# Optimization experiments

Hardware: AMD Instinct MI355X
Metric: run time of the kernel (lower is better)

Reference implementation:

```python
import jax, jax.numpy as jnp
import numpy as np

B, S, D = 4, 2048, 1024

def setup_inputs() -> dict:
    key = jax.random.key(0)
    k1, k2, k3, k4 = jax.random.split(key, 4)
    scale = 1.0 / np.sqrt(D)
    return {
        "X": jax.random.normal(k1, (B, S, D), dtype=jnp.float32),
        "W_Q": jax.random.normal(k2, (D, D), dtype=jnp.float32) * scale,
        "W_K": jax.random.normal(k3, (D, D), dtype=jnp.float32) * scale,
        "W_V": jax.random.normal(k4, (D, D), dtype=jnp.float32) * scale,
    }

def reference(X, W_Q, W_K, W_V):
    # nn.Linear computes X @ W.T; weights stored as [out, in]
    Q = jnp.einsum('bsd,ed->bse', X, W_Q)
    K = jnp.einsum('bsd,ed->bse', X, W_K)
    V = jnp.einsum('bsd,ed->bse', X, W_V)
    d_model = X.shape[-1]
    scores = jnp.einsum('bqd,bkd->bqk', Q, K) / jnp.sqrt(jnp.float32(d_model))
    S_len = X.shape[1]
    causal = jnp.tril(jnp.ones((S_len, S_len), dtype=bool))  # True = keep
    scores = jnp.where(causal[None, :, :], scores, -jnp.inf)
    attn = jax.nn.softmax(scores, axis=-1)
    return jnp.einsum('bqk,bkd->bqd', attn, V)
```

## Files before the change

kernel.cpp:

```cpp
#include <hip/hip_runtime.h>

typedef unsigned short u16;
typedef __attribute__((ext_vector_type(8))) short short8;
typedef __attribute__((ext_vector_type(4))) float floatx4;
typedef __attribute__((ext_vector_type(4))) unsigned short ushortx4;

#define BATCH 4
#define SEQ   2048
#define DMODEL 1024

__device__ __forceinline__ u16 f2bf(float f) {
  unsigned int u = __builtin_bit_cast(unsigned int, f);
  u = (u + 0x7FFFu + ((u >> 16) & 1u)) >> 16;
  return (u16)u;
}

typedef const __attribute__((address_space(1))) unsigned int as1_u32;
typedef __attribute__((address_space(3))) unsigned int as3_u32;

__device__ __forceinline__ void gload16(const void* gp, void* lp) {
  __builtin_amdgcn_global_load_lds((as1_u32*)gp, (as3_u32*)lp, 16, 0, 0);
}

#define CFENCE asm volatile("" ::: "memory")
#define LGKM0  do { asm volatile("s_waitcnt lgkmcnt(0)" ::: "memory"); \
                    __builtin_amdgcn_sched_barrier(0); } while (0)
#define VMC(n) asm volatile("s_waitcnt vmcnt(" #n ")" ::: "memory")
#define BAR    __builtin_amdgcn_s_barrier()
#define PRIO1  __builtin_amdgcn_s_setprio(1)
#define PRIO0  __builtin_amdgcn_s_setprio(0)

template<int NW, int STRIPE>
__device__ __forceinline__ void stage_unit(
    const u16* __restrict__ G, int ld, int org, int kt, int h,
    u16* region, int w, int l)
{
  constexpr int CPS = STRIPE / 16;
  const int lr = l >> 3, s = l & 7;
  #pragma unroll
  for (int i = 0; i < 2; ++i) {
    int c = i * NW + w;
    int R = (c / CPS) * STRIPE + h * (STRIPE / 2) + (c % CPS) * 8;
    const u16* src = G + (size_t)(org + R + lr) * ld + kt * 64 + ((s ^ lr) << 3);
    gload16(src, region + R * 64);
  }
}

template<int REP>
__device__ __forceinline__ short8 rdfrag(const u16* region, int wq, int m, int kh, int l) {
  int r = wq * (REP * 16) + m * 16 + (l & 15);
  int c = kh * 32 + ((l >> 4) << 3);
  return *(const short8*)(region + ((r * 64 + c) ^ ((r & 7) << 3)));
}

template<int WM, int WN, int MREP, int NREP>
__device__ __forceinline__ void gemm_core(
    const u16* __restrict__ A, int lda,
    const u16* __restrict__ B, int ldb,
    int m0, int n0, int NT, u16* lds,
    floatx4 (&acc)[MREP][NREP])
{
  constexpr int NW = WM * WN;
  constexpr int BM = WM * MREP * 16, BN = WN * NREP * 16;
  constexpr int ABUF = BM * 64;
  constexpr int BUFSZ = (BM + BN) * 64;
  constexpr int MH = MREP / 2, NH = NREP / 2;
  constexpr int SA = BM / WM, SB = BN / WN;

  const int tid = threadIdx.x;
  const int w = tid >> 6, l = tid & 63;
  const int wr = w / WN, wc = w % WN;

  u16* const bufp[2] = { lds, lds + BUFSZ };

  stage_unit<NW, SA>(A, lda, m0, 0, 0, bufp[0], w, l);
  stage_unit<NW, SB>(B, ldb, n0, 0, 0, bufp[0] + ABUF, w, l);
  stage_unit<NW, SB>(B, ldb, n0, 0, 1, bufp[0] + ABUF, w, l);
  stage_unit<NW, SA>(A, lda, m0, 0, 1, bufp[0], w, l);
  stage_unit<NW, SA>(A, lda, m0, 1, 0, bufp[1], w, l);
  stage_unit<NW, SB>(B, ldb, n0, 1, 0, bufp[1] + ABUF, w, l);
  stage_unit<NW, SB>(B, ldb, n0, 1, 1, bufp[1] + ABUF, w, l);
  VMC(6);
  BAR;
  CFENCE;

  for (int t = 0; t < NT; t += 2) {
    u16* c0 = bufp[t & 1];
    u16* c1 = bufp[(t + 1) & 1];
    const int t2 = (t + 2 < NT) ? t + 2 : NT - 1;
    const int t3 = (t + 3 < NT) ? t + 3 : NT - 1;

    short8 aLo[MH][2], aHi[MH][2], bLo[NH][2], bHi[NH][2];

    #pragma unroll
    for (int m = 0; m < MH; ++m)
      #pragma unroll
      for (int k = 0; k < 2; ++k) aLo[m][k] = rdfrag<MREP>(c0, wr, m, k, l);
    #pragma unroll
    for (int n = 0; n < NH; ++n)
      #pragma unroll
      for (int k = 0; k < 2; ++k) bLo[n][k] = rdfrag<NREP>(c0 + ABUF, wc, n, k, l);
    stage_unit<NW, SA>(A, lda, m0, t + 1, 1, c1, w, l);
    if constexpr (MH * 2 + NH * 2 >= 12) asm volatile("s_waitcnt lgkmcnt(8)" ::: "memory");
    BAR; LGKM0; PRIO1;
    #pragma unroll
    for (int m = 0; m < MH; ++m)
      #pragma unroll
      for (int n = 0; n < NH; ++n)
        #pragma unroll
        for (int k = 0; k < 2; ++k)
          acc[m][n] = __builtin_amdgcn_mfma_f32_16x16x32_bf16(aLo[m][k], bLo[n][k], acc[m][n], 0, 0, 0);
    PRIO0; BAR; CFENCE;

    #pragma unroll
    for (int n = 0; n < NH; ++n)
      #pragma unroll
      for (int k = 0; k < 2; ++k) bHi[n][k] = rdfrag<NREP>(c0 + ABUF, wc, n + NH, k, l);
    stage_unit<NW, SA>(A, lda, m0, t2, 0, c0, w, l);
    BAR; LGKM0; PRIO1;
    #pragma unroll
    for (int m = 0; m < MH; ++m)
      #pragma unroll
      for (int n = 0; n < NH; ++n)
        #pragma unroll
        for (int k = 0; k < 2; ++k)
          acc[m][n + NH] = __builtin_amdgcn_mfma_f32_16x16x32_bf16(aLo[m][k], bHi[n][k], acc[m][n + NH], 0, 0, 0);
    PRIO0; BAR; CFENCE;

    #pragma unroll
    for (int m = 0; m < MH; ++m)
      #pragma unroll
      for (int k = 0; k < 2; ++k) aHi[m][k] = rdfrag<MREP>(c0, wr, m + MH, k, l);
    stage_unit<NW, SB>(B, ldb, n0, t2, 0, c0 + ABUF, w, l);
    BAR; LGKM0; PRIO1;
    #pragma unroll
    for (int m = 0; m < MH; ++m)
      #pragma unroll
      for (int n = 0; n < NH; ++n)
        #pragma unroll
        for (int k = 0; k < 2; ++k)
          acc[m + MH][n + NH] = __builtin_amdgcn_mfma_f32_16x16x32_bf16(aHi[m][k], bHi[n][k], acc[m + MH][n + NH], 0, 0, 0);
    PRIO0; BAR; CFENCE;

    stage_unit<NW, SB>(B, ldb, n0, t2, 1, c0 + ABUF, w, l);
    VMC(6);
    BAR; PRIO1;
    #pragma unroll
    for (int m = 0; m < MH; ++m)
      #pragma unroll
      for (int n = 0; n < NH; ++n)
        #pragma unroll
        for (int k = 0; k < 2; ++k)
          acc[m + MH][n] = __builtin_amdgcn_mfma_f32_16x16x32_bf16(aHi[m][k], bLo[n][k], acc[m + MH][n], 0, 0, 0);
    PRIO0; BAR; CFENCE;

    #pragma unroll
    for (int m = 0; m < MH; ++m)
      #pragma unroll
      for (int k = 0; k < 2; ++k) aLo[m][k] = rdfrag<MREP>(c1, wr, m, k, l);
    #pragma unroll
    for (int n = 0; n < NH; ++n)
      #pragma unroll
      for (int k = 0; k < 2; ++k) bLo[n][k] = rdfrag<NREP>(c1 + ABUF, wc, n, k, l);
    stage_unit<NW, SA>(A, lda, m0, t2, 1, c0, w, l);
    if constexpr (MH * 2 + NH * 2 >= 12) asm volatile("s_waitcnt lgkmcnt(8)" ::: "memory");
    BAR; LGKM0; PRIO1;
    #pragma unroll
    for (int m = 0; m < MH; ++m)
      #pragma unroll
      for (int n = 0; n < NH; ++n)
        #pragma unroll
        for (int k = 0; k < 2; ++k)
          acc[m][n] = __builtin_amdgcn_mfma_f32_16x16x32_bf16(aLo[m][k], bLo[n][k], acc[m][n], 0, 0, 0);
    PRIO0; BAR; CFENCE;

    #pragma unroll
    for (int n = 0; n < NH; ++n)
      #pragma unroll
      for (int k = 0; k < 2; ++k) bHi[n][k] = rdfrag<NREP>(c1 + ABUF, wc, n + NH, k, l);
    stage_unit<NW, SA>(A, lda, m0, t3, 0, c1, w, l);
    BAR; LGKM0; PRIO1;
    #pragma unroll
    for (int m = 0; m < MH; ++m)
      #pragma unroll
      for (int n = 0; n < NH; ++n)
        #pragma unroll
        for (int k = 0; k < 2; ++k)
          acc[m][n + NH] = __builtin_amdgcn_mfma_f32_16x16x32_bf16(aLo[m][k], bHi[n][k], acc[m][n + NH], 0, 0, 0);
    PRIO0; BAR; CFENCE;

    #pragma unroll
    for (int m = 0; m < MH; ++m)
      #pragma unroll
      for (int k = 0; k < 2; ++k) aHi[m][k] = rdfrag<MREP>(c1, wr, m + MH, k, l);
    stage_unit<NW, SB>(B, ldb, n0, t3, 0, c1 + ABUF, w, l);
    BAR; LGKM0; PRIO1;
    #pragma unroll
    for (int m = 0; m < MH; ++m)
      #pragma unroll
      for (int n = 0; n < NH; ++n)
        #pragma unroll
        for (int k = 0; k < 2; ++k)
          acc[m + MH][n + NH] = __builtin_amdgcn_mfma_f32_16x16x32_bf16(aHi[m][k], bHi[n][k], acc[m + MH][n + NH], 0, 0, 0);
    PRIO0; BAR; CFENCE;

    stage_unit<NW, SB>(B, ldb, n0, t3, 1, c1 + ABUF, w, l);
    VMC(6);
    BAR; PRIO1;
    #pragma unroll
    for (int m = 0; m < MH; ++m)
      #pragma unroll
      for (int n = 0; n < NH; ++n)
        #pragma unroll
        for (int k = 0; k < 2; ++k)
          acc[m + MH][n] = __builtin_amdgcn_mfma_f32_16x16x32_bf16(aHi[m][k], bLo[n][k], acc[m + MH][n], 0, 0, 0);
    PRIO0; BAR; CFENCE;
  }
  VMC(0);
}

__global__ __launch_bounds__(256)
void convert_k(const float* __restrict__ X,
               const float* __restrict__ WQ,
               const float* __restrict__ WK,
               const float* __restrict__ WV,
               u16* __restrict__ Xb, u16* __restrict__ Wb)
{
  const int NX = (BATCH*SEQ*DMODEL) / 4;
  const int NW_ = (DMODEL*DMODEL) / 4;
  const int total = NX + 3*NW_;
  for (int i = blockIdx.x * 256 + threadIdx.x; i < total; i += gridDim.x * 256) {
    const float4* src; u16* dst; int j;
    if (i < NX) { src = (const float4*)X; j = i; dst = Xb; }
    else {
      int t = i - NX; int w = t / NW_; j = t - w * NW_;
      src = (const float4*)(w == 0 ? WQ : (w == 1 ? WK : WV));
      dst = Wb + (size_t)w * (DMODEL*DMODEL);
    }
    float4 v = src[j];
    ushortx4 p = { f2bf(v.x), f2bf(v.y), f2bf(v.z), f2bf(v.w) };
    *(ushortx4*)(dst + (size_t)j * 4) = p;
  }
}

__global__ __launch_bounds__(512, 2)
void qk256(const u16* __restrict__ Xb, const u16* __restrict__ Wb,
           u16* __restrict__ Q, u16* __restrict__ K)
{
  __shared__ __align__(16) u16 lds[2 * (256 + 256) * 64];
  const int id = blockIdx.x;
  const int sw = (id & 7) * 32 + (id >> 3);
  const int z = sw >> 7;
  const int rem = sw & 127;
  const int mt = rem >> 2, nt = rem & 3;
  const int m0 = mt * 256, n0 = nt * 256;

  floatx4 acc[8][4] = {};
  gemm_core<2, 4, 8, 4>(Xb, DMODEL, Wb + (size_t)z * DMODEL * DMODEL, DMODEL,
                        m0, n0, DMODEL / 64, lds, acc);

  const int l = threadIdx.x & 63, w = threadIdx.x >> 6;
  const int wr = w >> 2, wc = w & 3;
  const int row0 = m0 + wr * 128 + ((l >> 4) << 2);
  const int col0 = n0 + wc * 64 + (l & 15);
  u16* O = z ? K : Q;
  #pragma unroll
  for (int m = 0; m < 8; ++m)
    #pragma unroll
    for (int n = 0; n < 4; ++n)
      #pragma unroll
      for (int i = 0; i < 4; ++i)
        O[(size_t)(row0 + m*16 + i) * DMODEL + col0 + n*16] = f2bf(acc[m][n][i]);
}

__global__ __launch_bounds__(256, 2)
void v128(const u16* __restrict__ Xb, const u16* __restrict__ Wb,
          u16* __restrict__ Vt)
{
  __shared__ __align__(16) u16 lds[2 * (128 + 128) * 64];
  const int id = blockIdx.x;
  const int sw = (id & 7) * 64 + (id >> 3);
  const int mt = sw >> 3, nt = sw & 7;
  const int m0 = mt * 128, n0 = nt * 128;

  floatx4 acc[4][4] = {};
  gemm_core<2, 2, 4, 4>(Xb, DMODEL, Wb + (size_t)2 * DMODEL * DMODEL, DMODEL,
                        m0, n0, DMODEL / 64, lds, acc);

  const int l = threadIdx.x & 63, w = threadIdx.x >> 6;
  const int wr = w >> 1, wc = w & 1;
  const int row0 = m0 + wr * 64 + ((l >> 4) << 2);
  const int col0 = n0 + wc * 64 + (l & 15);
  #pragma unroll
  for (int m = 0; m < 4; ++m) {
    int gm = row0 + m*16;
    int b = gm >> 11, s = gm & (SEQ - 1);
    #pragma unroll
    for (int n = 0; n < 4; ++n) {
      int d = col0 + n*16;
      ushortx4 p = { f2bf(acc[m][n][0]), f2bf(acc[m][n][1]),
                     f2bf(acc[m][n][2]), f2bf(acc[m][n][3]) };
      *(ushortx4*)(Vt + ((size_t)b * DMODEL + d) * SEQ + s) = p;
    }
  }
}

__global__ __launch_bounds__(256, 2)
void scores128(const u16* __restrict__ Qb, const u16* __restrict__ Kb,
               float* __restrict__ Sc)
{
  __shared__ __align__(16) u16 lds[2 * (128 + 128) * 64];
  const int id = blockIdx.x;
  const int sw = (id & 7) * 68 + (id >> 3);
  const int b = sw / 136;
  const int t = sw % 136;
  int qt = 0;
  while ((qt + 1) * (qt + 2) / 2 <= t) ++qt;
  const int kt = t - qt * (qt + 1) / 2;
  const int m0 = qt * 128, n0 = kt * 128;

  const u16* Q = Qb + (size_t)b * SEQ * DMODEL;
  const u16* K = Kb + (size_t)b * SEQ * DMODEL;
  floatx4 acc[4][4] = {};
  gemm_core<2, 2, 4, 4>(Q, DMODEL, K, DMODEL, m0, n0, DMODEL / 64, lds, acc);

  float* S = Sc + (size_t)b * SEQ * SEQ;
  const int l = threadIdx.x & 63, w = threadIdx.x >> 6;
  const int wr = w >> 1, wc = w & 1;
  const int row0 = m0 + wr * 64 + ((l >> 4) << 2);
  const int col0 = n0 + wc * 64 + (l & 15);
  #pragma unroll
  for (int m = 0; m < 4; ++m)
    #pragma unroll
    for (int n = 0; n < 4; ++n)
      #pragma unroll
      for (int i = 0; i < 4; ++i)
        S[(size_t)(row0 + m*16 + i) * SEQ + col0 + n*16] = acc[m][n][i] * 0.03125f;
}

__global__ __launch_bounds__(256)
void softmax_k(float* __restrict__ Sc)
{
  __shared__ float buf[SEQ];
  __shared__ float red[4];
  const int rg = blockIdx.x;
  const int q = rg & (SEQ - 1);
  float* row = Sc + (size_t)rg * SEQ;
  u16* prow = (u16*)row;
  const int tid = threadIdx.x;
  const int lane = tid & 63, wave = tid >> 6;
  const int n = q + 1;
  const int kpad = ((q >> 8) + 1) << 8;

  float lmax = -3.4e38f;
  for (int k = tid; k < n; k += 256) {
    float v = row[k];
    buf[k] = v;
    lmax = fmaxf(lmax, v);
  }
  #pragma unroll
  for (int off = 32; off >= 1; off >>= 1)
    lmax = fmaxf(lmax, __shfl_xor(lmax, off));
  if (lane == 0) red[wave] = lmax;
  __syncthreads();
  const float rmax = fmaxf(fmaxf(red[0], red[1]), fmaxf(red[2], red[3]));
  __syncthreads();

  float lsum = 0.f;
  for (int k = tid; k < n; k += 256) {
    float e = __expf(buf[k] - rmax);
    buf[k] = e;
    lsum += e;
  }
  #pragma unroll
  for (int off = 32; off >= 1; off >>= 1)
    lsum += __shfl_xor(lsum, off);
  if (lane == 0) red[wave] = lsum;
  __syncthreads();
  const float inv = 1.f / (red[0] + red[1] + red[2] + red[3]);

  for (int k = tid; k < kpad; k += 256) {
    float p = (k < n) ? buf[k] * inv : 0.f;
    prow[k] = f2bf(p);
  }
}

__global__ __launch_bounds__(256, 2)
void out128(const float* __restrict__ Sc, const u16* __restrict__ Vt,
            float* __restrict__ Out)
{
  __shared__ __align__(16) u16 lds[2 * (128 + 128) * 64];
  const int id = blockIdx.x;
  const int j = id & 255;
  const int upper = id >> 8;
  const int qt = upper ? (15 - (j & 15)) : (j & 15);
  const int nt = (j >> 4) & 7;
  const int b  = (upper << 1) | (j >> 7);
  const int m0 = qt * 128, n0 = nt * 128;

  const u16* P = (const u16*)(Sc + (size_t)b * SEQ * SEQ);
  const u16* V = Vt + (size_t)b * DMODEL * SEQ;
  const int NT = (qt + 1) * 2;

  floatx4 acc[4][4] = {};
  gemm_core<2, 2, 4, 4>(P, 2 * SEQ, V, SEQ, m0, n0, NT, lds, acc);

  float* O = Out + (size_t)b * SEQ * DMODEL;
  const int l = threadIdx.x & 63, w = threadIdx.x >> 6;
  const int wr = w >> 1, wc = w & 1;
  const int row0 = m0 + wr * 64 + ((l >> 4) << 2);
  const int col0 = n0 + wc * 64 + (l & 15);
  #pragma unroll
  for (int m = 0; m < 4; ++m)
    #pragma unroll
    for (int n = 0; n < 4; ++n)
      #pragma unroll
      for (int i = 0; i < 4; ++i)
        O[(size_t)(row0 + m*16 + i) * DMODEL + col0 + n*16] = acc[m][n][i];
}

extern "C" void kernel_launch(void* const* d_in, const int* in_sizes, int n_in,
                              void* d_out, int out_size, void* d_ws, size_t ws_size,
                              hipStream_t stream)
{
  const float* X  = (const float*)d_in[0];
  const float* WQ = (const float*)d_in[1];
  const float* WK = (const float*)d_in[2];
  const float* WV = (const float*)d_in[3];
  float* Out = (float*)d_out;

  char* ws = (char*)d_ws;
  u16*   Xb = (u16*)(ws);
  u16*   Wb = (u16*)(ws + 16777216);
  u16*   Qb = (u16*)(ws + 23068672);
  u16*   Kb = (u16*)(ws + 39845888);
  u16*   Vt = (u16*)(ws + 56623104);
  float* Sc = (float*)(ws + 73400320);

  convert_k<<<dim3(2048), dim3(256), 0, stream>>>(X, WQ, WK, WV, Xb, Wb);
  qk256<<<dim3(256), dim3(512), 0, stream>>>(Xb, Wb, Qb, Kb);
  v128<<<dim3(512), dim3(256), 0, stream>>>(Xb, Wb, Vt);
  scores128<<<dim3(544), dim3(256), 0, stream>>>(Qb, Kb, Sc);
  softmax_k<<<dim3(BATCH * SEQ), dim3(256), 0, stream>>>(Sc);
  out128<<<dim3(512), dim3(256), 0, stream>>>(Sc, Vt, Out);
}
```

Before: 145.2 us.

## Merge V projection with scores GEMM, store scores in bf16, single-pass softmax

Merges the V projection and QK^T scores GEMMs into one launch of 1056 blocks, so they share a grid and one launch is removed. Scores are now written as bf16 instead of fp32, which halves the score-matrix traffic into and out of softmax. Softmax loads one 8-element vector per thread into registers instead of staging through LDS, and pads the causal row to 128 instead of 256. The QK projection switches to a new three-phase gemm_core variant with finer-grained prefetch and barriers. Rounding scores to bf16 before softmax lowers precision.

```diff
diff --git a/kernel.cpp b/kernel.cpp
--- a/kernel.cpp
+++ b/kernel.cpp
@@ -13,6 +13,10 @@
   unsigned int u = __builtin_bit_cast(unsigned int, f);
   u = (u + 0x7FFFu + ((u >> 16) & 1u)) >> 16;
   return (u16)u;
+}
+__device__ __forceinline__ float bf2f(u16 u) {
+  unsigned int v = ((unsigned int)u) << 16;
+  return __builtin_bit_cast(float, v);
 }
 
 typedef const __attribute__((address_space(1))) unsigned int as1_u32;
@@ -54,7 +58,113 @@
 }
 
 template<int WM, int WN, int MREP, int NREP>
-__device__ __forceinline__ void gemm_core(
+__device__ __forceinline__ void gemm_core3(
+    const u16* __restrict__ A, int lda,
+    const u16* __restrict__ B, int ldb,
+    int m0, int n0, int NT, u16* lds,
+    floatx4 (&acc)[MREP][NREP])
+{
+  constexpr int NW = WM * WN;
+  constexpr int BM = WM * MREP * 16, BN = WN * NREP * 16;
+  constexpr int ABUF = BM * 64;
+  constexpr int BUFSZ = (BM + BN) * 64;
+  constexpr int MH = MREP / 2, NH = NREP / 2;
+  constexpr int SA = BM / WM, SB = BN / WN;
+
+  const int tid = threadIdx.x;
+  const int w = tid >> 6, l = tid & 63;
+  const int wr = w / WN, wc = w % WN;
+
+  u16* buf0 = lds;
+  u16* buf1 = lds + BUFSZ;
+
+  stage_unit<NW, SA>(A, lda, m0, 0, 0, buf0, w, l);
+  stage_unit<NW, SB>(B, ldb, n0, 0, 0, buf0 + ABUF, w, l);
+  stage_unit<NW, SB>(B, ldb, n0, 0, 1, buf0 + ABUF, w, l);
+  stage_unit<NW, SA>(A, lda, m0, 0, 1, buf0, w, l);
+  stage_unit<NW, SA>(A, lda, m0, 1, 0, buf1, w, l);
+  stage_unit<NW, SB>(B, ldb, n0, 1, 0, buf1 + ABUF, w, l);
+  VMC(8);
+  BAR;
+  CFENCE;
+
+  for (int kt = 0; kt < NT; ++kt) {
+    u16* cur = (kt & 1) ? buf1 : buf0;
+    u16* oth = (kt & 1) ? buf0 : buf1;
+    const int t1 = (kt + 1 < NT) ? kt + 1 : NT - 1;
+    const int t2 = (kt + 2 < NT) ? kt + 2 : NT - 1;
+
+    short8 aLo[MH][2], aHi[MH][2], bLo[NH][2], bHi[NH][2];
+
+    #pragma unroll
+    for (int m = 0; m < MH; ++m)
+      #pragma unroll
+      for (int k = 0; k < 2; ++k) aLo[m][k] = rdfrag<MREP>(cur, wr, m, k, l);
+    #pragma unroll
+    for (int n = 0; n < NH; ++n)
+      #pragma unroll
+      for (int k = 0; k < 2; ++k) bLo[n][k] = rdfrag<NREP>(cur + ABUF, wc, n, k, l);
+    stage_unit<NW, SB>(B, ldb, n0, t1, 1, oth + ABUF, w, l);
+    stage_unit<NW, SA>(A, lda, m0, t1, 1, oth, w, l);
+    VMC(10);
+    LGKM0;
+    BAR;
+    CFENCE;
+    PRIO1;
+    #pragma unroll
+    for (int m = 0; m < MH; ++m)
+      #pragma unroll
+      for (int n = 0; n < NH; ++n)
+        #pragma unroll
+        for (int k = 0; k < 2; ++k)
+          acc[m][n] = __builtin_amdgcn_mfma_f32_16x16x32_bf16(aLo[m][k], bLo[n][k], acc[m][n], 0, 0, 0);
+    PRIO0;
+
+    #pragma unroll
+    for (int n = 0; n < NH; ++n)
+      #pragma unroll
+      for (int k = 0; k < 2; ++k) bHi[n][k] = rdfrag<NREP>(cur + ABUF, wc, n + NH, k, l);
+    stage_unit<NW, SA>(A, lda, m0, t2, 0, cur, w, l);
+    VMC(10);
+    LGKM0;
+    BAR;
+    CFENCE;
+    PRIO1;
+    #pragma unroll
+    for (int m = 0; m < MH; ++m)
+      #pragma unroll
+      for (int n = 0; n < NH; ++n)
+        #pragma unroll
+        for (int k = 0; k < 2; ++k)
+          acc[m][n + NH] = __builtin_amdgcn_mfma_f32_16x16x32_bf16(aLo[m][k], bHi[n][k], acc[m][n + NH], 0, 0, 0);
+    PRIO0;
+
+    #pragma unroll
+    for (int m = 0; m < MH; ++m)
+      #pragma unroll
+      for (int k = 0; k < 2; ++k) aHi[m][k] = rdfrag<MREP>(cur, wr, m + MH, k, l);
+    stage_unit<NW, SB>(B, ldb, n0, t2, 0, cur + ABUF, w, l);
+    VMC(8);
+    LGKM0;
+    BAR;
+    CFENCE;
+    PRIO1;
+    #pragma unroll
+    for (int m = 0; m < MH; ++m)
+      #pragma unroll
+      for (int n = 0; n < NH; ++n)
+        #pragma unroll
+        for (int k = 0; k < 2; ++k) {
+          acc[m + MH][n + NH] = __builtin_amdgcn_mfma_f32_16x16x32_bf16(aHi[m][k], bHi[n][k], acc[m + MH][n + NH], 0, 0, 0);
+          acc[m + MH][n] = __builtin_amdgcn_mfma_f32_16x16x32_bf16(aHi[m][k], bLo[n][k], acc[m + MH][n], 0, 0, 0);
+        }
+    PRIO0;
+  }
+  VMC(0);
+}
+
+template<int WM, int WN, int MREP, int NREP>
+__device__ __forceinline__ void gemm_core8(
     const u16* __restrict__ A, int lda,
     const u16* __restrict__ B, int ldb,
     int m0, int n0, int NT, u16* lds,
@@ -256,8 +366,8 @@
   const int m0 = mt * 256, n0 = nt * 256;
 
   floatx4 acc[8][4] = {};
-  gemm_core<2, 4, 8, 4>(Xb, DMODEL, Wb + (size_t)z * DMODEL * DMODEL, DMODEL,
-                        m0, n0, DMODEL / 64, lds, acc);
+  gemm_core3<2, 4, 8, 4>(Xb, DMODEL, Wb + (size_t)z * DMODEL * DMODEL, DMODEL,
+                         m0, n0, DMODEL / 64, lds, acc);
 
   const int l = threadIdx.x & 63, w = threadIdx.x >> 6;
   const int wr = w >> 2, wc = w & 3;
@@ -274,89 +384,88 @@
 }
 
 __global__ __launch_bounds__(256, 2)
-void v128(const u16* __restrict__ Xb, const u16* __restrict__ Wb,
-          u16* __restrict__ Vt)
+void sv128(const u16* __restrict__ Xb, const u16* __restrict__ Wb,
+           const u16* __restrict__ Qb, const u16* __restrict__ Kb,
+           u16* __restrict__ Sc, u16* __restrict__ Vt)
 {
   __shared__ __align__(16) u16 lds[2 * (128 + 128) * 64];
   const int id = blockIdx.x;
-  const int sw = (id & 7) * 64 + (id >> 3);
-  const int mt = sw >> 3, nt = sw & 7;
-  const int m0 = mt * 128, n0 = nt * 128;
+  const int sw = (id & 7) * 132 + (id >> 3);
+
+  const u16 *A, *B;
+  int m0, n0, b = 0;
+  bool is_s;
+  if (sw < 544) {
+    is_s = true;
+    b = sw / 136;
+    const int t = sw % 136;
+    int qt = 0;
+    while ((qt + 1) * (qt + 2) / 2 <= t) ++qt;
+    const int kt = t - qt * (qt + 1) / 2;
+    m0 = qt * 128; n0 = kt * 128;
+    A = Qb + (size_t)b * SEQ * DMODEL;
+    B = Kb + (size_t)b * SEQ * DMODEL;
+  } else {
+    is_s = false;
+    const int s = sw - 544;
+    m0 = (s >> 3) * 128; n0 = (s & 7) * 128;
+    A = Xb;
+    B = Wb + (size_t)2 * DMODEL * DMODEL;
+  }
 
   floatx4 acc[4][4] = {};
-  gemm_core<2, 2, 4, 4>(Xb, DMODEL, Wb + (size_t)2 * DMODEL * DMODEL, DMODEL,
-                        m0, n0, DMODEL / 64, lds, acc);
+  gemm_core8<2, 2, 4, 4>(A, DMODEL, B, DMODEL, m0, n0, DMODEL / 64, lds, acc);
 
   const int l = threadIdx.x & 63, w = threadIdx.x >> 6;
   const int wr = w >> 1, wc = w & 1;
   const int row0 = m0 + wr * 64 + ((l >> 4) << 2);
   const int col0 = n0 + wc * 64 + (l & 15);
-  #pragma unroll
-  for (int m = 0; m < 4; ++m) {
-    int gm = row0 + m*16;
-    int b = gm >> 11, s = gm & (SEQ - 1);
-    #pragma unroll
-    for (int n = 0; n < 4; ++n) {
-      int d = col0 + n*16;
-      ushortx4 p = { f2bf(acc[m][n][0]), f2bf(acc[m][n][1]),
-                     f2bf(acc[m][n][2]), f2bf(acc[m][n][3]) };
-      *(ushortx4*)(Vt + ((size_t)b * DMODEL + d) * SEQ + s) = p;
+
+  if (is_s) {
+    u16* S = Sc + (size_t)b * SEQ * SEQ;
+    #pragma unroll
+    for (int m = 0; m < 4; ++m)
+      #pragma unroll
+      for (int n = 0; n < 4; ++n)
+        #pragma unroll
+        for (int i = 0; i < 4; ++i)
+          S[(size_t)(row0 + m*16 + i) * SEQ + col0 + n*16] = f2bf(acc[m][n][i] * 0.03125f);
+  } else {
+    #pragma unroll
+    for (int m = 0; m < 4; ++m) {
+      int gm = row0 + m*16;
+      int bb = gm >> 11, s2 = gm & (SEQ - 1);
+      #pragma unroll
+      for (int n = 0; n < 4; ++n) {
+        int d = col0 + n*16;
+        ushortx4 p = { f2bf(acc[m][n][0]), f2bf(acc[m][n][1]),
+                       f2bf(acc[m][n][2]), f2bf(acc[m][n][3]) };
+        *(ushortx4*)(Vt + ((size_t)bb * DMODEL + d) * SEQ + s2) = p;
+      }
     }
   }
 }
 
-__global__ __launch_bounds__(256, 2)
-void scores128(const u16* __restrict__ Qb, const u16* __restrict__ Kb,
-               float* __restrict__ Sc)
-{
-  __shared__ __align__(16) u16 lds[2 * (128 + 128) * 64];
-  const int id = blockIdx.x;
-  const int sw = (id & 7) * 68 + (id >> 3);
-  const int b = sw / 136;
-  const int t = sw % 136;
-  int qt = 0;
-  while ((qt + 1) * (qt + 2) / 2 <= t) ++qt;
-  const int kt = t - qt * (qt + 1) / 2;
-  const int m0 = qt * 128, n0 = kt * 128;
-
-  const u16* Q = Qb + (size_t)b * SEQ * DMODEL;
-  const u16* K = Kb + (size_t)b * SEQ * DMODEL;
-  floatx4 acc[4][4] = {};
-  gemm_core<2, 2, 4, 4>(Q, DMODEL, K, DMODEL, m0, n0, DMODEL / 64, lds, acc);
-
-  float* S = Sc + (size_t)b * SEQ * SEQ;
-  const int l = threadIdx.x & 63, w = threadIdx.x >> 6;
-  const int wr = w >> 1, wc = w & 1;
-  const int row0 = m0 + wr * 64 + ((l >> 4) << 2);
-  const int col0 = n0 + wc * 64 + (l & 15);
-  #pragma unroll
-  for (int m = 0; m < 4; ++m)
-    #pragma unroll
-    for (int n = 0; n < 4; ++n)
-      #pragma unroll
-      for (int i = 0; i < 4; ++i)
-        S[(size_t)(row0 + m*16 + i) * SEQ + col0 + n*16] = acc[m][n][i] * 0.03125f;
-}
-
 __global__ __launch_bounds__(256)
-void softmax_k(float* __restrict__ Sc)
-{
-  __shared__ float buf[SEQ];
+void softmax1p(u16* __restrict__ Sc)
+{
   __shared__ float red[4];
   const int rg = blockIdx.x;
   const int q = rg & (SEQ - 1);
-  float* row = Sc + (size_t)rg * SEQ;
-  u16* prow = (u16*)row;
-  const int tid = threadIdx.x;
-  const int lane = tid & 63, wave = tid >> 6;
+  u16* row = Sc + (size_t)rg * SEQ;
+  const int t = threadIdx.x;
+  const int lane = t & 63, wave = t >> 6;
   const int n = q + 1;
-  const int kpad = ((q >> 8) + 1) << 8;
-
+  const int kpad = ((q >> 7) + 1) << 7;
+  const int k0 = t * 8;
+
+  short8 v8 = *(const short8*)(row + k0);
+  float f[8];
   float lmax = -3.4e38f;
-  for (int k = tid; k < n; k += 256) {
-    float v = row[k];
-    buf[k] = v;
-    lmax = fmaxf(lmax, v);
+  #pragma unroll
+  for (int j = 0; j < 8; ++j) {
+    f[j] = bf2f((u16)v8[j]);
+    if (k0 + j < n) lmax = fmaxf(lmax, f[j]);
   }
   #pragma unroll
   for (int off = 32; off >= 1; off >>= 1)
@@ -367,9 +476,10 @@
   __syncthreads();
 
   float lsum = 0.f;
-  for (int k = tid; k < n; k += 256) {
-    float e = __expf(buf[k] - rmax);
-    buf[k] = e;
+  #pragma unroll
+  for (int j = 0; j < 8; ++j) {
+    float e = (k0 + j < n) ? __expf(f[j] - rmax) : 0.f;
+    f[j] = e;
     lsum += e;
   }
   #pragma unroll
@@ -379,14 +489,16 @@
   __syncthreads();
   const float inv = 1.f / (red[0] + red[1] + red[2] + red[3]);
 
-  for (int k = tid; k < kpad; k += 256) {
-    float p = (k < n) ? buf[k] * inv : 0.f;
-    prow[k] = f2bf(p);
+  if (k0 < kpad) {
+    short8 o;
+    #pragma unroll
+    for (int j = 0; j < 8; ++j) o[j] = (short)f2bf(f[j] * inv);
+    *(short8*)(row + k0) = o;
   }
 }
 
 __global__ __launch_bounds__(256, 2)
-void out128(const float* __restrict__ Sc, const u16* __restrict__ Vt,
+void out128(const u16* __restrict__ Sc, const u16* __restrict__ Vt,
             float* __restrict__ Out)
 {
   __shared__ __align__(16) u16 lds[2 * (128 + 128) * 64];
@@ -398,12 +510,12 @@
   const int b  = (upper << 1) | (j >> 7);
   const int m0 = qt * 128, n0 = nt * 128;
 
-  const u16* P = (const u16*)(Sc + (size_t)b * SEQ * SEQ);
+  const u16* P = Sc + (size_t)b * SEQ * SEQ;
   const u16* V = Vt + (size_t)b * DMODEL * SEQ;
   const int NT = (qt + 1) * 2;
 
   floatx4 acc[4][4] = {};
-  gemm_core<2, 2, 4, 4>(P, 2 * SEQ, V, SEQ, m0, n0, NT, lds, acc);
+  gemm_core8<2, 2, 4, 4>(P, SEQ, V, SEQ, m0, n0, NT, lds, acc);
 
   float* O = Out + (size_t)b * SEQ * DMODEL;
   const int l = threadIdx.x & 63, w = threadIdx.x >> 6;
@@ -435,12 +547,11 @@
   u16*   Qb = (u16*)(ws + 23068672);
   u16*   Kb = (u16*)(ws + 39845888);
   u16*   Vt = (u16*)(ws + 56623104);
-  float* Sc = (float*)(ws + 73400320);
+  u16*   Sc = (u16*)(ws + 73400320);
 
   convert_k<<<dim3(2048), dim3(256), 0, stream>>>(X, WQ, WK, WV, Xb, Wb);
   qk256<<<dim3(256), dim3(512), 0, stream>>>(Xb, Wb, Qb, Kb);
-  v128<<<dim3(512), dim3(256), 0, stream>>>(Xb, Wb, Vt);
-  scores128<<<dim3(544), dim3(256), 0, stream>>>(Qb, Kb, Sc);
-  softmax_k<<<dim3(BATCH * SEQ), dim3(256), 0, stream>>>(Sc);
+  sv128<<<dim3(1056), dim3(256), 0, stream>>>(Xb, Wb, Qb, Kb, Sc, Vt);
+  softmax1p<<<dim3(BATCH * SEQ), dim3(256), 0, stream>>>(Sc);
   out128<<<dim3(512), dim3(256), 0, stream>>>(Sc, Vt, Out);
 }
```

Measured after the change: 134.9 us. -7.1%, faster.
